# Kernel tuning notes

Hardware: AMD Instinct MI355X
Metric: run time of the kernel (lower is better)

The kernel has to match this reference:

```python
import jax, jax.numpy as jnp
import numpy as np

ND, NG, E = 25000, 20000, 1_000_000
DIN_D, DIN_G, H, OUT = 128, 128, 128, 128


def setup_inputs() -> dict:
    key = jax.random.key(0)
    ks = jax.random.split(key, 12)

    def w(k, i, o):
        return jax.random.normal(k, (i, o), jnp.float32) / np.float32(np.sqrt(i))

    return {
        "x_disease": jax.random.normal(ks[0], (ND, DIN_D), jnp.float32),
        "x_gene": jax.random.normal(ks[1], (NG, DIN_G), jnp.float32),
        "src": jax.random.randint(ks[2], (E,), 0, ND, dtype=jnp.int32),  # disease endpoint
        "dst": jax.random.randint(ks[3], (E,), 0, NG, dtype=jnp.int32),  # gene endpoint
        # layer 1, relation disease->gene: lin_l acts on aggregated disease feats, lin_r on gene feats
        "w1_dg_l": w(ks[4], DIN_D, H), "b1_dg": jnp.zeros((H,), jnp.float32), "w1_dg_r": w(ks[5], DIN_G, H),
        # layer 1, relation gene->disease (reverse edges)
        "w1_gd_l": w(ks[6], DIN_G, H), "b1_gd": jnp.zeros((H,), jnp.float32), "w1_gd_r": w(ks[7], DIN_D, H),
        # layer 2
        "w2_dg_l": w(ks[8], H, OUT), "b2_dg": jnp.zeros((OUT,), jnp.float32), "w2_dg_r": w(ks[9], H, OUT),
        "w2_gd_l": w(ks[10], H, OUT), "b2_gd": jnp.zeros((OUT,), jnp.float32), "w2_gd_r": w(ks[11], H, OUT),
    }


def _sage(x_src, x_dst, e_src, e_dst, n_dst, W_l, b_l, W_r):
    """Bipartite SAGEConv: lin_l(mean of source neighbors) + lin_r(x_dst)."""
    msg = x_src[e_src]                                         # [E, d] gather
    s = jax.ops.segment_sum(msg, e_dst, num_segments=n_dst)    # [n_dst, d]
    cnt = jax.ops.segment_sum(jnp.ones((e_dst.shape[0],), x_src.dtype),
                              e_dst, num_segments=n_dst)
    mean = s / jnp.maximum(cnt, 1.0)[:, None]                  # isolated nodes -> 0
    return mean @ W_l + b_l + x_dst @ W_r


def reference(x_disease, x_gene, src, dst,
              w1_dg_l, b1_dg, w1_dg_r, w1_gd_l, b1_gd, w1_gd_r,
              w2_dg_l, b2_dg, w2_dg_r, w2_gd_l, b2_gd, w2_gd_r):
    # HeteroConv aggr='sum': each node type receives from exactly one relation here,
    # so the cross-relation sum is the single relation output.
    g1 = _sage(x_disease, x_gene, src, dst, NG, w1_dg_l, b1_dg, w1_dg_r)   # gene <- disease
    d1 = _sage(x_gene, x_disease, dst, src, ND, w1_gd_l, b1_gd, w1_gd_r)   # disease <- gene (rev)
    g2 = _sage(d1, g1, src, dst, NG, w2_dg_l, b2_dg, w2_dg_r)
    d2 = _sage(g1, d1, dst, src, ND, w2_gd_l, b2_gd, w2_gd_r)
    return d2, g2
```

## Files before the change

kernel.cpp:

```cpp
#include <hip/hip_runtime.h>
#include <hip/hip_fp16.h>

#define ND 25000
#define NG 20000
#define NTOT (ND + NG)
#define NBLK 128
#define PREPB 1024
#define NSB 176
#define AGG_SLOTS 1563
#define AGG_GRID (8 * AGG_SLOTS)

typedef _Float16 half8 __attribute__((ext_vector_type(8)));
typedef float f32x4 __attribute__((ext_vector_type(4)));
typedef float f32x2 __attribute__((ext_vector_type(2)));

#define OFF_CNT    0ull
#define OFF_ROW    180224ull
#define OFF_PARTD  360704ull
#define OFF_PARTG  6760704ull
#define OFF_COL    11880704ull
#define OFF_WSW    15880704ull
#define OFF_XDH    16142848ull
#define OFF_XGH    22542848ull
#define OFF_X8D    27662848ull
#define OFF_X8G    30862848ull
#define OFF_MDH    33422848ull
#define OFF_MGH    39822848ull
#define OFF_D1H    44942848ull
#define OFF_G1H    51342848ull
#define OFF_D18    56462848ull
#define OFF_G18    59662848ull

struct WPtrs { const float* w[8]; };

__global__ __launch_bounds__(256) void prep_hist(const float* __restrict__ xd,
                                                 const float* __restrict__ xg,
                                                 __half* __restrict__ ydh,
                                                 __half* __restrict__ ygh,
                                                 unsigned char* __restrict__ y8d,
                                                 unsigned char* __restrict__ y8g,
                                                 WPtrs wp, _Float16* __restrict__ wsw,
                                                 const int* __restrict__ src,
                                                 const int* __restrict__ dst,
                                                 unsigned short* __restrict__ partD,
                                                 unsigned short* __restrict__ partG,
                                                 unsigned int* __restrict__ flags, int E) {
    __shared__ unsigned int h[12544];
    int bx = blockIdx.x, t = threadIdx.x;
    if (bx < 2 * NBLK) {
        bool isD = bx < NBLK;
        int bb = isD ? bx : bx - NBLK;
        const int* key = isD ? src : dst;
        int nw = isD ? (ND / 2) : (NG / 2);
        for (int i = t; i < nw; i += 256) h[i] = 0;
        __syncthreads();
        int e0 = (int)(((long long)E * bb) / NBLK);
        int e1 = (int)(((long long)E * (bb + 1)) / NBLK);
        for (int e = e0 + t; e < e1; e += 256) {
            int k = key[e];
            atomicAdd(&h[k >> 1], 1u << ((k & 1) * 16));
        }
        __syncthreads();
        unsigned int* po = (unsigned int*)((isD ? partD : partG) + (size_t)bb * (isD ? ND : NG));
        for (int i = t; i < nw; i += 256) po[i] = h[i];
        return;
    }
    int pb = bx - 2 * NBLK;
    if (pb < 8) {
        const float* W = wp.w[pb];
        _Float16* o = wsw + (size_t)pb * 16384;
        for (int rep = 0; rep < 8; ++rep) {
            int slot = rep * 256 + t;
            int lane = slot & 63, grp = slot >> 6;
            int kc = grp & 3, ntile = grp >> 2;
            int nn = ntile * 16 + (lane & 15);
            int kb = kc * 32 + (lane >> 4) * 8;
            half8 v;
#pragma unroll
            for (int j = 0; j < 8; ++j) v[j] = (_Float16)W[(size_t)(kb + j) * 128 + nn];
            *(half8*)(o + (size_t)slot * 8) = v;
        }
    } else if (pb == 8 && t < NSB) {
        flags[t] = 0u;
    }
    const int ndq = ND * 32;
    const int tot = ndq + NG * 32;
    for (int i = pb * 256 + t; i < tot; i += PREPB * 256) {
        const float* x;
        __half* y;
        unsigned char* y8;
        int idx;
        if (i < ndq) { x = xd; y = ydh; y8 = y8d; idx = i; }
        else         { x = xg; y = ygh; y8 = y8g; idx = i - ndq; }
        float4 v = ((const float4*)x)[idx];
        ((__half2*)y)[idx * 2 + 0] = __floats2half2_rn(v.x, v.y);
        ((__half2*)y)[idx * 2 + 1] = __floats2half2_rn(v.z, v.w);
        int p8 = __builtin_amdgcn_cvt_pk_fp8_f32(v.x, v.y, 0, false);
        p8 = __builtin_amdgcn_cvt_pk_fp8_f32(v.z, v.w, p8, true);
        ((int*)y8)[idx] = p8;
    }
}

__global__ __launch_bounds__(256) void scanall(unsigned short* __restrict__ partD,
                                               unsigned short* __restrict__ partG,
                                               int* __restrict__ row,
                                               unsigned int* __restrict__ flags, int E) {
    __shared__ int sd[256];
    __shared__ int sbase;
    int t = threadIdx.x, bid = blockIdx.x;
    int k = bid * 256 + t;
    int run = 0;
    if (k < NTOT) {
        unsigned short* part;
        int nb, kk;
        if (k < ND) { part = partD; nb = ND; kk = k; }
        else        { part = partG; nb = NG; kk = k - ND; }
#pragma unroll 8
        for (int b = 0; b < NBLK; ++b) {
            size_t idx = (size_t)b * nb + kk;
            int v = part[idx];
            part[idx] = (unsigned short)run;
            run += v;
        }
    }
    int tsum = run;
    sd[t] = tsum;
    __syncthreads();
    for (int off = 1; off < 256; off <<= 1) {
        int x = (t >= off) ? sd[t - off] : 0;
        __syncthreads();
        sd[t] += x;
        __syncthreads();
    }
    if (t == 0) {
        unsigned int agg = (unsigned int)sd[255] + 1u;
        __hip_atomic_store(&flags[bid], agg, __ATOMIC_RELEASE, __HIP_MEMORY_SCOPE_AGENT);
    }
    if (t < 64) {
        int s = 0;
        for (int i = t; i < bid; i += 64) {
            unsigned int v;
            do {
                v = __hip_atomic_load(&flags[i], __ATOMIC_ACQUIRE, __HIP_MEMORY_SCOPE_AGENT);
            } while (v == 0u);
            s += (int)v - 1;
        }
#pragma unroll
        for (int off = 1; off < 64; off <<= 1) s += __shfl_xor(s, off, 64);
        if (t == 0) sbase = s;
    }
    __syncthreads();
    int base = sbase;
    if (k < NTOT) row[k] = base + sd[t] - tsum;
    if (bid == 0 && t == 0) row[NTOT] = 2 * E;
}

__global__ __launch_bounds__(256) void fill2(const int* __restrict__ src,
                                             const int* __restrict__ dst,
                                             const int* __restrict__ row,
                                             const unsigned short* __restrict__ partD,
                                             const unsigned short* __restrict__ partG,
                                             unsigned short* __restrict__ col, int E) {
    __shared__ unsigned int h[12544];
    int t = threadIdx.x, b = blockIdx.x;
    bool isD = b < NBLK;
    int bb = isD ? b : b - NBLK;
    const int* key = isD ? src : dst;
    const int* val = isD ? dst : src;
    const int* rowp = isD ? row : row + ND;
    int nw = isD ? (ND / 2) : (NG / 2);
    const unsigned int* pi =
        (const unsigned int*)((isD ? partD : partG) + (size_t)bb * (isD ? ND : NG));
    for (int i = t; i < nw; i += 256) h[i] = pi[i];
    __syncthreads();
    int e0 = (int)(((long long)E * bb) / NBLK);
    int e1 = (int)(((long long)E * (bb + 1)) / NBLK);
    for (int e = e0 + t; e < e1; e += 256) {
        int k = key[e];
        int v = val[e];
        unsigned int old = atomicAdd(&h[k >> 1], 1u << ((k & 1) * 16));
        int rank = (old >> ((k & 1) * 16)) & 0xffff;
        col[rowp[k] + rank] = (unsigned short)v;
    }
}

__global__ __launch_bounds__(256, 8) void agg8m(const unsigned char* __restrict__ Xg,
                                                const unsigned char* __restrict__ Xd,
                                                const int* __restrict__ row,
                                                const unsigned short* __restrict__ col,
                                                __half* __restrict__ outd,
                                                __half* __restrict__ outg) {
    int wid = threadIdx.x >> 6, lane = threadIdx.x & 63;
    int bid = blockIdx.x;
    int xcd = bid & 7, slot = bid >> 3;
    const unsigned char* X;
    _Float16* out;
    int node, nloc;
    if (xcd < 4) {
        int db = slot * 4 + xcd;
        node = db * 4 + wid;
        if (node >= ND) return;
        X = Xg; out = (_Float16*)outd; nloc = node;
    } else {
        int gb = slot * 4 + (xcd - 4);
        int gn = gb * 4 + wid;
        if (gn >= NG) return;
        node = ND + gn;
        X = Xd; out = (_Float16*)outg; nloc = gn;
    }
    int b = row[node], e = row[node + 1];
    int g = lane >> 3, f = lane & 7;
    float acc[16];
#pragma unroll
    for (int k = 0; k < 16; ++k) acc[k] = 0.f;
    int j = b + g;
    for (; j + 8 < e; j += 16) {
        int c0 = col[j], c1 = col[j + 8];
        int4 w0 = *(const int4*)(X + (size_t)c0 * 128 + f * 16);
        int4 w1 = *(const int4*)(X + (size_t)c1 * 128 + f * 16);
        const int* wa = (const int*)&w0;
        const int* wb = (const int*)&w1;
#pragma unroll
        for (int q = 0; q < 4; ++q) {
            f32x2 l0 = __builtin_amdgcn_cvt_pk_f32_fp8(wa[q], false);
            f32x2 h0 = __builtin_amdgcn_cvt_pk_f32_fp8(wa[q], true);
            f32x2 l1 = __builtin_amdgcn_cvt_pk_f32_fp8(wb[q], false);
            f32x2 h1 = __builtin_amdgcn_cvt_pk_f32_fp8(wb[q], true);
            acc[q * 4 + 0] += l0[0] + l1[0];
            acc[q * 4 + 1] += l0[1] + l1[1];
            acc[q * 4 + 2] += h0[0] + h1[0];
            acc[q * 4 + 3] += h0[1] + h1[1];
        }
    }
    if (j < e) {
        int c = col[j];
        int4 w = *(const int4*)(X + (size_t)c * 128 + f * 16);
        const int* wa = (const int*)&w;
#pragma unroll
        for (int q = 0; q < 4; ++q) {
            f32x2 l = __builtin_amdgcn_cvt_pk_f32_fp8(wa[q], false);
            f32x2 h = __builtin_amdgcn_cvt_pk_f32_fp8(wa[q], true);
            acc[q * 4 + 0] += l[0];
            acc[q * 4 + 1] += l[1];
            acc[q * 4 + 2] += h[0];
            acc[q * 4 + 3] += h[1];
        }
    }
#pragma unroll
    for (int k = 0; k < 16; ++k) {
        acc[k] += __shfl_xor(acc[k], 8, 64);
        acc[k] += __shfl_xor(acc[k], 16, 64);
        acc[k] += __shfl_xor(acc[k], 32, 64);
    }
    if (g == 0) {
        int deg = e - b;
        float r = 1.0f / (float)(deg > 0 ? deg : 1);
        half8 o0, o1;
#pragma unroll
        for (int k = 0; k < 8; ++k) o0[k] = (_Float16)(acc[k] * r);
#pragma unroll
        for (int k = 0; k < 8; ++k) o1[k] = (_Float16)(acc[8 + k] * r);
        _Float16* op = out + (size_t)nloc * 128 + f * 16;
        *(half8*)op = o0;
        *(half8*)(op + 8) = o1;
    }
}

struct GemmDual {
    const __half *A1d, *A2d, *A1g, *A2g;
    const _Float16 *W1d, *W2d, *W1g, *W2g;
    const float *biasd, *biasg;
    float *Yfd, *Yfg;
    __half *Yhd, *Yhg;
    unsigned char *Y8d, *Y8g;
};
__global__ __launch_bounds__(256) void gemm2(GemmDual p, int nblkD, int layer) {
    int bx = blockIdx.x;
    bool isD = bx < nblkD;
    const __half* A1 = isD ? p.A1d : p.A1g;
    const __half* A2 = isD ? p.A2d : p.A2g;
    const _Float16* W1 = isD ? p.W1d : p.W1g;
    const _Float16* W2 = isD ? p.W2d : p.W2g;
    const float* bias = isD ? p.biasd : p.biasg;
    float* Yf = isD ? p.Yfd : p.Yfg;
    __half* Yh = isD ? p.Yhd : p.Yhg;
    unsigned char* Y8 = isD ? p.Y8d : p.Y8g;
    int n = isD ? ND : NG, b0 = isD ? bx : bx - nblkD;
    int t = threadIdx.x;
    int wave = t >> 6, lane = t & 63;
    int row0 = b0 * 64 + wave * 16;
    if (row0 >= n) return;
    int m = lane & 15, quad = lane >> 4;
    int arow = row0 + m;
    if (arow >= n) arow = n - 1;
    const _Float16* a1p = (const _Float16*)A1 + (size_t)arow * 128 + quad * 8;
    const _Float16* a2p = (const _Float16*)A2 + (size_t)arow * 128 + quad * 8;
    half8 a1[4], a2[4];
#pragma unroll
    for (int kc = 0; kc < 4; ++kc) {
        a1[kc] = *(const half8*)(a1p + kc * 32);
        a2[kc] = *(const half8*)(a2p + kc * 32);
    }
#pragma unroll
    for (int ntile = 0; ntile < 8; ++ntile) {
        f32x4 acc = {0.f, 0.f, 0.f, 0.f};
#pragma unroll
        for (int kc = 0; kc < 4; ++kc) {
            half8 b1 = *(const half8*)(W1 + (size_t)((ntile * 4 + kc) * 64 + lane) * 8);
            acc = __builtin_amdgcn_mfma_f32_16x16x32_f16(a1[kc], b1, acc, 0, 0, 0);
            half8 b2 = *(const half8*)(W2 + (size_t)((ntile * 4 + kc) * 64 + lane) * 8);
            acc = __builtin_amdgcn_mfma_f32_16x16x32_f16(a2[kc], b2, acc, 0, 0, 0);
        }
        int colx = ntile * 16 + m;
        float bb = bias[colx];
#pragma unroll
        for (int r = 0; r < 4; ++r) {
            int rr = row0 + quad * 4 + r;
            if (rr < n) {
                float v = acc[r] + bb;
                if (layer == 2) {
                    Yf[(size_t)rr * 128 + colx] = v;
                } else {
                    Yh[(size_t)rr * 128 + colx] = __float2half(v);
                    int p8 = __builtin_amdgcn_cvt_pk_fp8_f32(v, v, 0, false);
                    Y8[(size_t)rr * 128 + colx] = (unsigned char)(p8 & 0xff);
                }
            }
        }
    }
}

extern "C" void kernel_launch(void* const* d_in, const int* in_sizes, int n_in,
                              void* d_out, int out_size, void* d_ws, size_t ws_size,
                              hipStream_t stream) {
    const float* x_d = (const float*)d_in[0];
    const float* x_g = (const float*)d_in[1];
    const int*   src = (const int*)d_in[2];
    const int*   dst = (const int*)d_in[3];
    float* out = (float*)d_out;

    char* ws = (char*)d_ws;
    unsigned int*   flags = (unsigned int*)(ws + OFF_CNT);
    int*            row   = (int*)(ws + OFF_ROW);
    unsigned short* partD = (unsigned short*)(ws + OFF_PARTD);
    unsigned short* partG = (unsigned short*)(ws + OFF_PARTG);
    unsigned short* col   = (unsigned short*)(ws + OFF_COL);
    _Float16*       wsw   = (_Float16*)(ws + OFF_WSW);
    __half*         xd_h  = (__half*)(ws + OFF_XDH);
    __half*         xg_h  = (__half*)(ws + OFF_XGH);
    unsigned char*  x8d   = (unsigned char*)(ws + OFF_X8D);
    unsigned char*  x8g   = (unsigned char*)(ws + OFF_X8G);
    __half*         md_h  = (__half*)(ws + OFF_MDH);
    __half*         mg_h  = (__half*)(ws + OFF_MGH);
    __half*         d1_h  = (__half*)(ws + OFF_D1H);
    __half*         g1_h  = (__half*)(ws + OFF_G1H);
    unsigned char*  d1_8  = (unsigned char*)(ws + OFF_D18);
    unsigned char*  g1_8  = (unsigned char*)(ws + OFF_G18);

    const int E = in_sizes[2];
    const int nblkD = (ND + 63) / 64;
    const int nblkG = (NG + 63) / 64;

    WPtrs wp;
    wp.w[0] = (const float*)d_in[4];
    wp.w[1] = (const float*)d_in[6];
    wp.w[2] = (const float*)d_in[7];
    wp.w[3] = (const float*)d_in[9];
    wp.w[4] = (const float*)d_in[10];
    wp.w[5] = (const float*)d_in[12];
    wp.w[6] = (const float*)d_in[13];
    wp.w[7] = (const float*)d_in[15];
    const float* b1_dg = (const float*)d_in[5];
    const float* b1_gd = (const float*)d_in[8];
    const float* b2_dg = (const float*)d_in[11];
    const float* b2_gd = (const float*)d_in[14];

    prep_hist<<<2 * NBLK + PREPB, 256, 0, stream>>>(x_d, x_g, xd_h, xg_h, x8d, x8g,
                                                    wp, wsw, src, dst, partD, partG, flags, E);
    scanall<<<NSB, 256, 0, stream>>>(partD, partG, row, flags, E);
    fill2<<<2 * NBLK, 256, 0, stream>>>(src, dst, row, partD, partG, col, E);

    agg8m<<<AGG_GRID, 256, 0, stream>>>(x8g, x8d, row, col, md_h, mg_h);
    GemmDual g1p;
    g1p.A1d = md_h; g1p.A2d = xd_h; g1p.W1d = wsw + 2 * 16384; g1p.W2d = wsw + 3 * 16384;
    g1p.biasd = b1_gd; g1p.Yfd = nullptr; g1p.Yhd = d1_h; g1p.Y8d = d1_8;
    g1p.A1g = mg_h; g1p.A2g = xg_h; g1p.W1g = wsw + 0 * 16384; g1p.W2g = wsw + 1 * 16384;
    g1p.biasg = b1_dg; g1p.Yfg = nullptr; g1p.Yhg = g1_h; g1p.Y8g = g1_8;
    gemm2<<<nblkD + nblkG, 256, 0, stream>>>(g1p, nblkD, 1);

    agg8m<<<AGG_GRID, 256, 0, stream>>>(g1_8, d1_8, row, col, md_h, mg_h);
    GemmDual g2p;
    g2p.A1d = md_h; g2p.A2d = d1_h; g2p.W1d = wsw + 6 * 16384; g2p.W2d = wsw + 7 * 16384;
    g2p.biasd = b2_gd; g2p.Yfd = out; g2p.Yhd = nullptr; g2p.Y8d = nullptr;
    g2p.A1g = mg_h; g2p.A2g = g1_h; g2p.W1g = wsw + 4 * 16384; g2p.W2g = wsw + 5 * 16384;
    g2p.biasg = b2_dg; g2p.Yfg = out + (size_t)ND * 128; g2p.Yhg = nullptr; g2p.Y8g = nullptr;
    gemm2<<<nblkD + nblkG, 256, 0, stream>>>(g2p, nblkD, 2);
}
```

Measured before the change: 252.4 us.

## Fuse pipeline into two persistent cooperative kernels with grid-wide syncs

Merges the seven launches (histogram/prep, scan, fill, two aggregations, two GEMMs) into two cooperative persistent kernels separated by grid.sync barriers. Aggregation becomes a grid-stride loop over nodes instead of one block per node group. The aim is to cut kernel launch gaps and tail effects between stages. The cost is a fixed grid size bounded by occupancy, which may lower parallelism, add grid-barrier overhead, and leave some blocks idle during GEMM phases; a non-cooperative fallback path is kept.

```diff
diff --git a/kernel.cpp b/kernel.cpp
--- a/kernel.cpp
+++ b/kernel.cpp
@@ -1,14 +1,17 @@
 #include <hip/hip_runtime.h>
 #include <hip/hip_fp16.h>
+#include <hip/hip_cooperative_groups.h>
+
+namespace cg = cooperative_groups;
 
 #define ND 25000
 #define NG 20000
 #define NTOT (ND + NG)
 #define NBLK 128
-#define PREPB 1024
 #define NSB 176
-#define AGG_SLOTS 1563
-#define AGG_GRID (8 * AGG_SLOTS)
+#define NBD 391
+#define NBG 313
+#define NBT (NBD + NBG)
 
 typedef _Float16 half8 __attribute__((ext_vector_type(8)));
 typedef float f32x4 __attribute__((ext_vector_type(4)));
@@ -31,90 +34,96 @@
 #define OFF_D18    56462848ull
 #define OFF_G18    59662848ull
 
-struct WPtrs { const float* w[8]; };
-
-__global__ __launch_bounds__(256) void prep_hist(const float* __restrict__ xd,
-                                                 const float* __restrict__ xg,
-                                                 __half* __restrict__ ydh,
-                                                 __half* __restrict__ ygh,
-                                                 unsigned char* __restrict__ y8d,
-                                                 unsigned char* __restrict__ y8g,
-                                                 WPtrs wp, _Float16* __restrict__ wsw,
-                                                 const int* __restrict__ src,
-                                                 const int* __restrict__ dst,
-                                                 unsigned short* __restrict__ partD,
-                                                 unsigned short* __restrict__ partG,
-                                                 unsigned int* __restrict__ flags, int E) {
-    __shared__ unsigned int h[12544];
+struct PrepP {
+    const float *xd, *xg;
+    __half *ydh, *ygh;
+    unsigned char *y8d, *y8g;
+    const float* w[8];
+    _Float16* wsw;
+    const int *src, *dst;
+    unsigned short *partD, *partG;
+    unsigned int* flags;
+    int* row;
+    unsigned short* col;
+    int E;
+};
+
+struct MainP {
+    const unsigned char *x8d, *x8g;
+    unsigned char *d18, *g18;
+    const __half *xdh, *xgh;
+    __half *mdh, *mgh, *d1h, *g1h;
+    const _Float16* wsw;
+    const float *b1dg, *b1gd, *b2dg, *b2gd;
+    float* out;
+    const int* row;
+    const unsigned short* col;
+};
+
+
+__device__ void phase_hist_prep(const PrepP& p, unsigned int* h) {
     int bx = blockIdx.x, t = threadIdx.x;
     if (bx < 2 * NBLK) {
         bool isD = bx < NBLK;
         int bb = isD ? bx : bx - NBLK;
-        const int* key = isD ? src : dst;
+        const int* key = isD ? p.src : p.dst;
         int nw = isD ? (ND / 2) : (NG / 2);
         for (int i = t; i < nw; i += 256) h[i] = 0;
         __syncthreads();
-        int e0 = (int)(((long long)E * bb) / NBLK);
-        int e1 = (int)(((long long)E * (bb + 1)) / NBLK);
+        int e0 = (int)(((long long)p.E * bb) / NBLK);
+        int e1 = (int)(((long long)p.E * (bb + 1)) / NBLK);
         for (int e = e0 + t; e < e1; e += 256) {
             int k = key[e];
             atomicAdd(&h[k >> 1], 1u << ((k & 1) * 16));
         }
         __syncthreads();
-        unsigned int* po = (unsigned int*)((isD ? partD : partG) + (size_t)bb * (isD ? ND : NG));
+        unsigned int* po = (unsigned int*)((isD ? p.partD : p.partG) + (size_t)bb * (isD ? ND : NG));
         for (int i = t; i < nw; i += 256) po[i] = h[i];
-        return;
-    }
-    int pb = bx - 2 * NBLK;
-    if (pb < 8) {
-        const float* W = wp.w[pb];
-        _Float16* o = wsw + (size_t)pb * 16384;
-        for (int rep = 0; rep < 8; ++rep) {
-            int slot = rep * 256 + t;
-            int lane = slot & 63, grp = slot >> 6;
-            int kc = grp & 3, ntile = grp >> 2;
-            int nn = ntile * 16 + (lane & 15);
-            int kb = kc * 32 + (lane >> 4) * 8;
-            half8 v;
-#pragma unroll
-            for (int j = 0; j < 8; ++j) v[j] = (_Float16)W[(size_t)(kb + j) * 128 + nn];
-            *(half8*)(o + (size_t)slot * 8) = v;
-        }
-    } else if (pb == 8 && t < NSB) {
-        flags[t] = 0u;
-    }
-    const int ndq = ND * 32;
-    const int tot = ndq + NG * 32;
-    for (int i = pb * 256 + t; i < tot; i += PREPB * 256) {
-        const float* x;
-        __half* y;
-        unsigned char* y8;
-        int idx;
-        if (i < ndq) { x = xd; y = ydh; y8 = y8d; idx = i; }
-        else         { x = xg; y = ygh; y8 = y8g; idx = i - ndq; }
-        float4 v = ((const float4*)x)[idx];
-        ((__half2*)y)[idx * 2 + 0] = __floats2half2_rn(v.x, v.y);
-        ((__half2*)y)[idx * 2 + 1] = __floats2half2_rn(v.z, v.w);
-        int p8 = __builtin_amdgcn_cvt_pk_fp8_f32(v.x, v.y, 0, false);
-        p8 = __builtin_amdgcn_cvt_pk_fp8_f32(v.z, v.w, p8, true);
-        ((int*)y8)[idx] = p8;
-    }
-}
-
-__global__ __launch_bounds__(256) void scanall(unsigned short* __restrict__ partD,
-                                               unsigned short* __restrict__ partG,
-                                               int* __restrict__ row,
-                                               unsigned int* __restrict__ flags, int E) {
-    __shared__ int sd[256];
-    __shared__ int sbase;
+    } else {
+        int pb = bx - 2 * NBLK;
+        int ncb = gridDim.x - 2 * NBLK;
+        if (pb < 8) {
+            const float* W = p.w[pb];
+            _Float16* o = p.wsw + (size_t)pb * 16384;
+            for (int rep = 0; rep < 8; ++rep) {
+                int slot = rep * 256 + t;
+                int lane = slot & 63, grp = slot >> 6;
+                int kc = grp & 3, ntile = grp >> 2;
+                int nn = ntile * 16 + (lane & 15);
+                int kb = kc * 32 + (lane >> 4) * 8;
+                half8 v;
+#pragma unroll
+                for (int j = 0; j < 8; ++j) v[j] = (_Float16)W[(size_t)(kb + j) * 128 + nn];
+                *(half8*)(o + (size_t)slot * 8) = v;
+            }
+        } else if (pb == 8 && t < NSB) {
+            p.flags[t] = 0u;
+        }
+        const int ndq = ND * 32;
+        const int tot = ndq + NG * 32;
+        for (int i = pb * 256 + t; i < tot; i += ncb * 256) {
+            const float* x; __half* y; unsigned char* y8; int idx;
+            if (i < ndq) { x = p.xd; y = p.ydh; y8 = p.y8d; idx = i; }
+            else         { x = p.xg; y = p.ygh; y8 = p.y8g; idx = i - ndq; }
+            float4 v = ((const float4*)x)[idx];
+            ((__half2*)y)[idx * 2 + 0] = __floats2half2_rn(v.x, v.y);
+            ((__half2*)y)[idx * 2 + 1] = __floats2half2_rn(v.z, v.w);
+            int p8 = __builtin_amdgcn_cvt_pk_fp8_f32(v.x, v.y, 0, false);
+            p8 = __builtin_amdgcn_cvt_pk_fp8_f32(v.z, v.w, p8, true);
+            ((int*)y8)[idx] = p8;
+        }
+    }
+}
+
+__device__ void phase_scan(const PrepP& p, int* sd, int* sbase_p) {
     int t = threadIdx.x, bid = blockIdx.x;
     int k = bid * 256 + t;
     int run = 0;
     if (k < NTOT) {
         unsigned short* part;
         int nb, kk;
-        if (k < ND) { part = partD; nb = ND; kk = k; }
-        else        { part = partG; nb = NG; kk = k - ND; }
+        if (k < ND) { part = p.partD; nb = ND; kk = k; }
+        else        { part = p.partG; nb = NG; kk = k - ND; }
 #pragma unroll 8
         for (int b = 0; b < NBLK; ++b) {
             size_t idx = (size_t)b * nb + kk;
@@ -134,80 +143,54 @@
     }
     if (t == 0) {
         unsigned int agg = (unsigned int)sd[255] + 1u;
-        __hip_atomic_store(&flags[bid], agg, __ATOMIC_RELEASE, __HIP_MEMORY_SCOPE_AGENT);
+        __hip_atomic_store(&p.flags[bid], agg, __ATOMIC_RELEASE, __HIP_MEMORY_SCOPE_AGENT);
     }
     if (t < 64) {
         int s = 0;
         for (int i = t; i < bid; i += 64) {
             unsigned int v;
             do {
-                v = __hip_atomic_load(&flags[i], __ATOMIC_ACQUIRE, __HIP_MEMORY_SCOPE_AGENT);
+                v = __hip_atomic_load(&p.flags[i], __ATOMIC_ACQUIRE, __HIP_MEMORY_SCOPE_AGENT);
             } while (v == 0u);
             s += (int)v - 1;
         }
 #pragma unroll
         for (int off = 1; off < 64; off <<= 1) s += __shfl_xor(s, off, 64);
-        if (t == 0) sbase = s;
+        if (t == 0) *sbase_p = s;
     }
     __syncthreads();
-    int base = sbase;
-    if (k < NTOT) row[k] = base + sd[t] - tsum;
-    if (bid == 0 && t == 0) row[NTOT] = 2 * E;
-}
-
-__global__ __launch_bounds__(256) void fill2(const int* __restrict__ src,
-                                             const int* __restrict__ dst,
-                                             const int* __restrict__ row,
-                                             const unsigned short* __restrict__ partD,
-                                             const unsigned short* __restrict__ partG,
-                                             unsigned short* __restrict__ col, int E) {
-    __shared__ unsigned int h[12544];
+    int base = *sbase_p;
+    if (k < NTOT) p.row[k] = base + sd[t] - tsum;
+    if (bid == 0 && t == 0) p.row[NTOT] = 2 * p.E;
+}
+
+__device__ void phase_fill(const PrepP& p, unsigned int* h) {
     int t = threadIdx.x, b = blockIdx.x;
     bool isD = b < NBLK;
     int bb = isD ? b : b - NBLK;
-    const int* key = isD ? src : dst;
-    const int* val = isD ? dst : src;
-    const int* rowp = isD ? row : row + ND;
+    const int* key = isD ? p.src : p.dst;
+    const int* val = isD ? p.dst : p.src;
+    const int* rowp = isD ? p.row : p.row + ND;
     int nw = isD ? (ND / 2) : (NG / 2);
     const unsigned int* pi =
-        (const unsigned int*)((isD ? partD : partG) + (size_t)bb * (isD ? ND : NG));
+        (const unsigned int*)((isD ? p.partD : p.partG) + (size_t)bb * (isD ? ND : NG));
     for (int i = t; i < nw; i += 256) h[i] = pi[i];
     __syncthreads();
-    int e0 = (int)(((long long)E * bb) / NBLK);
-    int e1 = (int)(((long long)E * (bb + 1)) / NBLK);
+    int e0 = (int)(((long long)p.E * bb) / NBLK);
+    int e1 = (int)(((long long)p.E * (bb + 1)) / NBLK);
     for (int e = e0 + t; e < e1; e += 256) {
         int k = key[e];
         int v = val[e];
         unsigned int old = atomicAdd(&h[k >> 1], 1u << ((k & 1) * 16));
         int rank = (old >> ((k & 1) * 16)) & 0xffff;
-        col[rowp[k] + rank] = (unsigned short)v;
-    }
-}
-
-__global__ __launch_bounds__(256, 8) void agg8m(const unsigned char* __restrict__ Xg,
-                                                const unsigned char* __restrict__ Xd,
-                                                const int* __restrict__ row,
-                                                const unsigned short* __restrict__ col,
-                                                __half* __restrict__ outd,
-                                                __half* __restrict__ outg) {
-    int wid = threadIdx.x >> 6, lane = threadIdx.x & 63;
-    int bid = blockIdx.x;
-    int xcd = bid & 7, slot = bid >> 3;
-    const unsigned char* X;
-    _Float16* out;
-    int node, nloc;
-    if (xcd < 4) {
-        int db = slot * 4 + xcd;
-        node = db * 4 + wid;
-        if (node >= ND) return;
-        X = Xg; out = (_Float16*)outd; nloc = node;
-    } else {
-        int gb = slot * 4 + (xcd - 4);
-        int gn = gb * 4 + wid;
-        if (gn >= NG) return;
-        node = ND + gn;
-        X = Xd; out = (_Float16*)outg; nloc = gn;
-    }
+        p.col[rowp[k] + rank] = (unsigned short)v;
+    }
+}
+
+__device__ __forceinline__ void agg_one(const unsigned char* __restrict__ X,
+                                        const int* __restrict__ row,
+                                        const unsigned short* __restrict__ col,
+                                        int node, _Float16* __restrict__ op0, int lane) {
     int b = row[node], e = row[node + 1];
     int g = lane >> 3, f = lane & 7;
     float acc[16];
@@ -260,32 +243,34 @@
         for (int k = 0; k < 8; ++k) o0[k] = (_Float16)(acc[k] * r);
 #pragma unroll
         for (int k = 0; k < 8; ++k) o1[k] = (_Float16)(acc[8 + k] * r);
-        _Float16* op = out + (size_t)nloc * 128 + f * 16;
-        *(half8*)op = o0;
-        *(half8*)(op + 8) = o1;
-    }
-}
-
-struct GemmDual {
-    const __half *A1d, *A2d, *A1g, *A2g;
-    const _Float16 *W1d, *W2d, *W1g, *W2g;
-    const float *biasd, *biasg;
-    float *Yfd, *Yfg;
-    __half *Yhd, *Yhg;
-    unsigned char *Y8d, *Y8g;
-};
-__global__ __launch_bounds__(256) void gemm2(GemmDual p, int nblkD, int layer) {
-    int bx = blockIdx.x;
-    bool isD = bx < nblkD;
-    const __half* A1 = isD ? p.A1d : p.A1g;
-    const __half* A2 = isD ? p.A2d : p.A2g;
-    const _Float16* W1 = isD ? p.W1d : p.W1g;
-    const _Float16* W2 = isD ? p.W2d : p.W2g;
-    const float* bias = isD ? p.biasd : p.biasg;
-    float* Yf = isD ? p.Yfd : p.Yfg;
-    __half* Yh = isD ? p.Yhd : p.Yhg;
-    unsigned char* Y8 = isD ? p.Y8d : p.Y8g;
-    int n = isD ? ND : NG, b0 = isD ? bx : bx - nblkD;
+        *(half8*)(op0 + f * 16) = o0;
+        *(half8*)(op0 + f * 16 + 8) = o1;
+    }
+}
+
+__device__ void aggp(const unsigned char* __restrict__ Xg, const unsigned char* __restrict__ Xd,
+                     const int* __restrict__ row, const unsigned short* __restrict__ col,
+                     __half* __restrict__ outd, __half* __restrict__ outg) {
+    int wid = threadIdx.x >> 6, lane = threadIdx.x & 63;
+    int bid = blockIdx.x;
+    int xcd = bid & 7, slot = bid >> 3;
+    int stride = gridDim.x * 2;
+    if (xcd < 4) {
+        int widx = (slot * 4 + xcd) * 4 + wid;
+        for (int nd = widx; nd < ND; nd += stride)
+            agg_one(Xg, row, col, nd, (_Float16*)outd + (size_t)nd * 128, lane);
+    } else {
+        int widx = (slot * 4 + (xcd - 4)) * 4 + wid;
+        for (int gn = widx; gn < NG; gn += stride)
+            agg_one(Xd, row, col, ND + gn, (_Float16*)outg + (size_t)gn * 128, lane);
+    }
+}
+
+__device__ void gemm_tile(const __half* __restrict__ A1, const __half* __restrict__ A2,
+                          const _Float16* __restrict__ W1, const _Float16* __restrict__ W2,
+                          const float* __restrict__ bias,
+                          float* __restrict__ Yf, __half* __restrict__ Yh,
+                          unsigned char* __restrict__ Y8, int n, int b0, int layer) {
     int t = threadIdx.x;
     int wave = t >> 6, lane = t & 63;
     int row0 = b0 * 64 + wave * 16;
@@ -330,6 +315,79 @@
     }
 }
 
+__device__ void gemm_sel(const MainP& p, int layer) {
+    int bx = blockIdx.x;
+    bool isD = bx < NBD;
+    int n = isD ? ND : NG, b0 = isD ? bx : bx - NBD;
+    const __half* A1 = isD ? p.mdh : p.mgh;
+    const __half* A2;
+    const _Float16 *W1, *W2;
+    const float* bias;
+    float* Yf = nullptr;
+    __half* Yh = nullptr;
+    unsigned char* Y8 = nullptr;
+    if (layer == 1) {
+        A2 = isD ? p.xdh : p.xgh;
+        W1 = p.wsw + (size_t)(isD ? 2 : 0) * 16384;
+        W2 = p.wsw + (size_t)(isD ? 3 : 1) * 16384;
+        bias = isD ? p.b1gd : p.b1dg;
+        Yh = isD ? p.d1h : p.g1h;
+        Y8 = isD ? p.d18 : p.g18;
+    } else {
+        A2 = isD ? p.d1h : p.g1h;
+        W1 = p.wsw + (size_t)(isD ? 6 : 4) * 16384;
+        W2 = p.wsw + (size_t)(isD ? 7 : 5) * 16384;
+        bias = isD ? p.b2gd : p.b2dg;
+        Yf = isD ? p.out : p.out + (size_t)ND * 128;
+    }
+    gemm_tile(A1, A2, W1, W2, bias, Yf, Yh, Y8, n, b0, layer);
+}
+
+
+__global__ __launch_bounds__(256, 3) void csrprep(PrepP p) {
+    __shared__ unsigned int h[12544];
+    __shared__ int sbase;
+    cg::grid_group grid = cg::this_grid();
+    phase_hist_prep(p, h);
+    grid.sync();
+    if (blockIdx.x < NSB) phase_scan(p, (int*)h, &sbase);
+    grid.sync();
+    if (blockIdx.x < 2 * NBLK) phase_fill(p, h);
+}
+
+__global__ __launch_bounds__(256, 8) void mainfused(MainP p) {
+    cg::grid_group grid = cg::this_grid();
+    aggp(p.x8g, p.x8d, p.row, p.col, p.mdh, p.mgh);
+    grid.sync();
+    if (blockIdx.x < NBT) gemm_sel(p, 1);
+    grid.sync();
+    aggp(p.g18, p.d18, p.row, p.col, p.mdh, p.mgh);
+    grid.sync();
+    if (blockIdx.x < NBT) gemm_sel(p, 2);
+}
+
+
+__global__ __launch_bounds__(256) void k_prep(PrepP p) {
+    __shared__ unsigned int h[12544];
+    phase_hist_prep(p, h);
+}
+__global__ __launch_bounds__(256) void k_scan(PrepP p) {
+    __shared__ int sd[256];
+    __shared__ int sbase;
+    phase_scan(p, sd, &sbase);
+}
+__global__ __launch_bounds__(256) void k_fill(PrepP p) {
+    __shared__ unsigned int h[12544];
+    if (blockIdx.x < 2 * NBLK) phase_fill(p, h);
+}
+__global__ __launch_bounds__(256, 8) void k_agg(MainP p, int layer) {
+    if (layer == 1) aggp(p.x8g, p.x8d, p.row, p.col, p.mdh, p.mgh);
+    else            aggp(p.g18, p.d18, p.row, p.col, p.mdh, p.mgh);
+}
+__global__ __launch_bounds__(256) void k_gemm(MainP p, int layer) {
+    if (blockIdx.x < NBT) gemm_sel(p, layer);
+}
+
 extern "C" void kernel_launch(void* const* d_in, const int* in_sizes, int n_in,
                               void* d_out, int out_size, void* d_ws, size_t ws_size,
                               hipStream_t stream) {
@@ -340,59 +398,85 @@
     float* out = (float*)d_out;
 
     char* ws = (char*)d_ws;
-    unsigned int*   flags = (unsigned int*)(ws + OFF_CNT);
-    int*            row   = (int*)(ws + OFF_ROW);
-    unsigned short* partD = (unsigned short*)(ws + OFF_PARTD);
-    unsigned short* partG = (unsigned short*)(ws + OFF_PARTG);
-    unsigned short* col   = (unsigned short*)(ws + OFF_COL);
-    _Float16*       wsw   = (_Float16*)(ws + OFF_WSW);
-    __half*         xd_h  = (__half*)(ws + OFF_XDH);
-    __half*         xg_h  = (__half*)(ws + OFF_XGH);
-    unsigned char*  x8d   = (unsigned char*)(ws + OFF_X8D);
-    unsigned char*  x8g   = (unsigned char*)(ws + OFF_X8G);
-    __half*         md_h  = (__half*)(ws + OFF_MDH);
-    __half*         mg_h  = (__half*)(ws + OFF_MGH);
-    __half*         d1_h  = (__half*)(ws + OFF_D1H);
-    __half*         g1_h  = (__half*)(ws + OFF_G1H);
-    unsigned char*  d1_8  = (unsigned char*)(ws + OFF_D18);
-    unsigned char*  g1_8  = (unsigned char*)(ws + OFF_G18);
-
-    const int E = in_sizes[2];
-    const int nblkD = (ND + 63) / 64;
-    const int nblkG = (NG + 63) / 64;
-
-    WPtrs wp;
-    wp.w[0] = (const float*)d_in[4];
-    wp.w[1] = (const float*)d_in[6];
-    wp.w[2] = (const float*)d_in[7];
-    wp.w[3] = (const float*)d_in[9];
-    wp.w[4] = (const float*)d_in[10];
-    wp.w[5] = (const float*)d_in[12];
-    wp.w[6] = (const float*)d_in[13];
-    wp.w[7] = (const float*)d_in[15];
-    const float* b1_dg = (const float*)d_in[5];
-    const float* b1_gd = (const float*)d_in[8];
-    const float* b2_dg = (const float*)d_in[11];
-    const float* b2_gd = (const float*)d_in[14];
-
-    prep_hist<<<2 * NBLK + PREPB, 256, 0, stream>>>(x_d, x_g, xd_h, xg_h, x8d, x8g,
-                                                    wp, wsw, src, dst, partD, partG, flags, E);
-    scanall<<<NSB, 256, 0, stream>>>(partD, partG, row, flags, E);
-    fill2<<<2 * NBLK, 256, 0, stream>>>(src, dst, row, partD, partG, col, E);
-
-    agg8m<<<AGG_GRID, 256, 0, stream>>>(x8g, x8d, row, col, md_h, mg_h);
-    GemmDual g1p;
-    g1p.A1d = md_h; g1p.A2d = xd_h; g1p.W1d = wsw + 2 * 16384; g1p.W2d = wsw + 3 * 16384;
-    g1p.biasd = b1_gd; g1p.Yfd = nullptr; g1p.Yhd = d1_h; g1p.Y8d = d1_8;
-    g1p.A1g = mg_h; g1p.A2g = xg_h; g1p.W1g = wsw + 0 * 16384; g1p.W2g = wsw + 1 * 16384;
-    g1p.biasg = b1_dg; g1p.Yfg = nullptr; g1p.Yhg = g1_h; g1p.Y8g = g1_8;
-    gemm2<<<nblkD + nblkG, 256, 0, stream>>>(g1p, nblkD, 1);
-
-    agg8m<<<AGG_GRID, 256, 0, stream>>>(g1_8, d1_8, row, col, md_h, mg_h);
-    GemmDual g2p;
-    g2p.A1d = md_h; g2p.A2d = d1_h; g2p.W1d = wsw + 6 * 16384; g2p.W2d = wsw + 7 * 16384;
-    g2p.biasd = b2_gd; g2p.Yfd = out; g2p.Yhd = nullptr; g2p.Y8d = nullptr;
-    g2p.A1g = mg_h; g2p.A2g = g1_h; g2p.W1g = wsw + 4 * 16384; g2p.W2g = wsw + 5 * 16384;
-    g2p.biasg = b2_dg; g2p.Yfg = out + (size_t)ND * 128; g2p.Yhg = nullptr; g2p.Y8g = nullptr;
-    gemm2<<<nblkD + nblkG, 256, 0, stream>>>(g2p, nblkD, 2);
-}
+    PrepP pp;
+    pp.xd = x_d; pp.xg = x_g;
+    pp.ydh = (__half*)(ws + OFF_XDH); pp.ygh = (__half*)(ws + OFF_XGH);
+    pp.y8d = (unsigned char*)(ws + OFF_X8D); pp.y8g = (unsigned char*)(ws + OFF_X8G);
+    pp.w[0] = (const float*)d_in[4];
+    pp.w[1] = (const float*)d_in[6];
+    pp.w[2] = (const float*)d_in[7];
+    pp.w[3] = (const float*)d_in[9];
+    pp.w[4] = (const float*)d_in[10];
+    pp.w[5] = (const float*)d_in[12];
+    pp.w[6] = (const float*)d_in[13];
+    pp.w[7] = (const float*)d_in[15];
+    pp.wsw = (_Float16*)(ws + OFF_WSW);
+    pp.src = src; pp.dst = dst;
+    pp.partD = (unsigned short*)(ws + OFF_PARTD);
+    pp.partG = (unsigned short*)(ws + OFF_PARTG);
+    pp.flags = (unsigned int*)(ws + OFF_CNT);
+    pp.row = (int*)(ws + OFF_ROW);
+    pp.col = (unsigned short*)(ws + OFF_COL);
+    pp.E = in_sizes[2];
+
+    MainP mp;
+    mp.x8d = (const unsigned char*)(ws + OFF_X8D);
+    mp.x8g = (const unsigned char*)(ws + OFF_X8G);
+    mp.d18 = (unsigned char*)(ws + OFF_D18);
+    mp.g18 = (unsigned char*)(ws + OFF_G18);
+    mp.xdh = (const __half*)(ws + OFF_XDH);
+    mp.xgh = (const __half*)(ws + OFF_XGH);
+    mp.mdh = (__half*)(ws + OFF_MDH);
+    mp.mgh = (__half*)(ws + OFF_MGH);
+    mp.d1h = (__half*)(ws + OFF_D1H);
+    mp.g1h = (__half*)(ws + OFF_G1H);
+    mp.wsw = (const _Float16*)(ws + OFF_WSW);
+    mp.b1dg = (const float*)d_in[5];
+    mp.b1gd = (const float*)d_in[8];
+    mp.b2dg = (const float*)d_in[11];
+    mp.b2gd = (const float*)d_in[14];
+    mp.out = out;
+    mp.row = (const int*)(ws + OFF_ROW);
+    mp.col = (const unsigned short*)(ws + OFF_COL);
+
+    static int coop = -1, gA = 0, gB = 0;
+    if (coop < 0) {
+        int ca = 0, dev = 0;
+        hipGetDevice(&dev);
+        hipDeviceGetAttribute(&ca, hipDeviceAttributeCooperativeLaunch, dev);
+        if (ca) {
+            int mA = 0, mB = 0;
+            hipOccupancyMaxActiveBlocksPerMultiprocessor(&mA, csrprep, 256, 0);
+            hipOccupancyMaxActiveBlocksPerMultiprocessor(&mB, mainfused, 256, 0);
+            hipDeviceProp_t prop;
+            hipGetDeviceProperties(&prop, dev);
+            int ncu = prop.multiProcessorCount;
+            gA = mA * ncu; if (gA > 768) gA = 768;
+            gB = (mB * ncu) & ~7; if (gB > 2048) gB = 2048;
+            coop = (gA >= 2 * NBLK + 9 && gB >= NBT) ? 1 : 0;
+        } else {
+            coop = 0;
+        }
+    }
+
+    if (coop) {
+        void* aA[] = { (void*)&pp };
+        void* aB[] = { (void*)&mp };
+        hipError_t e1 = hipLaunchCooperativeKernel((const void*)csrprep, dim3(gA), dim3(256),
+                                                   aA, 0, stream);
+        hipError_t e2 = (e1 == hipSuccess)
+            ? hipLaunchCooperativeKernel((const void*)mainfused, dim3(gB), dim3(256),
+                                         aB, 0, stream)
+            : e1;
+        if (e1 == hipSuccess && e2 == hipSuccess) return;
+        coop = 0;
+    }
+
+    k_prep<<<2 * NBLK + 1024, 256, 0, stream>>>(pp);
+    k_scan<<<NSB, 256, 0, stream>>>(pp);
+    k_fill<<<2 * NBLK, 256, 0, stream>>>(pp);
+    k_agg<<<2048, 256, 0, stream>>>(mp, 1);
+    k_gemm<<<NBT, 256, 0, stream>>>(mp, 1);
+    k_agg<<<2048, 256, 0, stream>>>(mp, 2);
+    k_gemm<<<NBT, 256, 0, stream>>>(mp, 2);
+}
```

Result: slower. 912.8 us (+261.6%).

## Replace per-block histogram CSR build with global atomic counts and fused scan-fill

Applied to the files above, without the earlier changes.

Removes the per-block partial histograms (128 blocks × nodes of ushort partials) and their serial scan. Degrees are now counted with global atomics, and a single kernel scans them and then fills col through global atomic cursors after a grid-wide barrier. This cuts large partial-buffer traffic and one launch, but adds global atomic contention. It also makes the within-row neighbor order nondeterministic. The grid barrier relies on all 1024 blocks being co-resident.

```diff
diff --git a/kernel.cpp b/kernel.cpp
--- a/kernel.cpp
+++ b/kernel.cpp
@@ -4,9 +4,10 @@
 #define ND 25000
 #define NG 20000
 #define NTOT (ND + NG)
-#define NBLK 128
+#define HB 128
 #define PREPB 1024
 #define NSB 176
+#define CFB 1024
 #define AGG_SLOTS 1563
 #define AGG_GRID (8 * AGG_SLOTS)
 
@@ -16,8 +17,8 @@
 
 #define OFF_CNT    0ull
 #define OFF_ROW    180224ull
-#define OFF_PARTD  360704ull
-#define OFF_PARTG  6760704ull
+#define OFF_FLG    360704ull
+#define OFF_POS    361728ull
 #define OFF_COL    11880704ull
 #define OFF_WSW    15880704ull
 #define OFF_XDH    16142848ull
@@ -33,6 +34,13 @@
 
 struct WPtrs { const float* w[8]; };
 
+__global__ __launch_bounds__(256) void zerok(int* __restrict__ cnt,
+                                             unsigned int* __restrict__ flags) {
+    int i = blockIdx.x * 256 + threadIdx.x;
+    for (int k = i; k < NTOT; k += gridDim.x * 256) cnt[k] = 0;
+    if (i <= NSB) flags[i] = 0u;
+}
+
 __global__ __launch_bounds__(256) void prep_hist(const float* __restrict__ xd,
                                                  const float* __restrict__ xg,
                                                  __half* __restrict__ ydh,
@@ -42,30 +50,18 @@
                                                  WPtrs wp, _Float16* __restrict__ wsw,
                                                  const int* __restrict__ src,
                                                  const int* __restrict__ dst,
-                                                 unsigned short* __restrict__ partD,
-                                                 unsigned short* __restrict__ partG,
-                                                 unsigned int* __restrict__ flags, int E) {
-    __shared__ unsigned int h[12544];
+                                                 int* __restrict__ cnt, int E) {
     int bx = blockIdx.x, t = threadIdx.x;
-    if (bx < 2 * NBLK) {
-        bool isD = bx < NBLK;
-        int bb = isD ? bx : bx - NBLK;
-        const int* key = isD ? src : dst;
-        int nw = isD ? (ND / 2) : (NG / 2);
-        for (int i = t; i < nw; i += 256) h[i] = 0;
-        __syncthreads();
-        int e0 = (int)(((long long)E * bb) / NBLK);
-        int e1 = (int)(((long long)E * (bb + 1)) / NBLK);
+    if (bx < HB) {
+        int e0 = (int)(((long long)E * bx) / HB);
+        int e1 = (int)(((long long)E * (bx + 1)) / HB);
         for (int e = e0 + t; e < e1; e += 256) {
-            int k = key[e];
-            atomicAdd(&h[k >> 1], 1u << ((k & 1) * 16));
-        }
-        __syncthreads();
-        unsigned int* po = (unsigned int*)((isD ? partD : partG) + (size_t)bb * (isD ? ND : NG));
-        for (int i = t; i < nw; i += 256) po[i] = h[i];
+            atomicAdd(&cnt[src[e]], 1);
+            atomicAdd(&cnt[ND + dst[e]], 1);
+        }
         return;
     }
-    int pb = bx - 2 * NBLK;
+    int pb = bx - HB;
     if (pb < 8) {
         const float* W = wp.w[pb];
         _Float16* o = wsw + (size_t)pb * 16384;
@@ -80,8 +76,6 @@
             for (int j = 0; j < 8; ++j) v[j] = (_Float16)W[(size_t)(kb + j) * 128 + nn];
             *(half8*)(o + (size_t)slot * 8) = v;
         }
-    } else if (pb == 8 && t < NSB) {
-        flags[t] = 0u;
     }
     const int ndq = ND * 32;
     const int tot = ndq + NG * 32;
@@ -101,86 +95,68 @@
     }
 }
 
-__global__ __launch_bounds__(256) void scanall(unsigned short* __restrict__ partD,
-                                               unsigned short* __restrict__ partG,
-                                               int* __restrict__ row,
-                                               unsigned int* __restrict__ flags, int E) {
+__global__ __launch_bounds__(256) void csrfin(const int* __restrict__ cnt,
+                                              int* __restrict__ row,
+                                              int* __restrict__ pos,
+                                              unsigned int* __restrict__ flags,
+                                              const int* __restrict__ src,
+                                              const int* __restrict__ dst,
+                                              unsigned short* __restrict__ col, int E) {
     __shared__ int sd[256];
     __shared__ int sbase;
     int t = threadIdx.x, bid = blockIdx.x;
-    int k = bid * 256 + t;
-    int run = 0;
-    if (k < NTOT) {
-        unsigned short* part;
-        int nb, kk;
-        if (k < ND) { part = partD; nb = ND; kk = k; }
-        else        { part = partG; nb = NG; kk = k - ND; }
-#pragma unroll 8
-        for (int b = 0; b < NBLK; ++b) {
-            size_t idx = (size_t)b * nb + kk;
-            int v = part[idx];
-            part[idx] = (unsigned short)run;
-            run += v;
-        }
-    }
-    int tsum = run;
-    sd[t] = tsum;
+    if (bid < NSB) {
+        int k = bid * 256 + t;
+        int tsum = (k < NTOT) ? cnt[k] : 0;
+        sd[t] = tsum;
+        __syncthreads();
+        for (int off = 1; off < 256; off <<= 1) {
+            int x = (t >= off) ? sd[t - off] : 0;
+            __syncthreads();
+            sd[t] += x;
+            __syncthreads();
+        }
+        if (t == 0) {
+            __hip_atomic_store(&flags[bid], (unsigned int)sd[255] + 1u,
+                               __ATOMIC_RELEASE, __HIP_MEMORY_SCOPE_AGENT);
+        }
+        if (t < 64) {
+            int s = 0;
+            for (int i = t; i < bid; i += 64) {
+                unsigned int v;
+                do {
+                    v = __hip_atomic_load(&flags[i], __ATOMIC_ACQUIRE, __HIP_MEMORY_SCOPE_AGENT);
+                } while (v == 0u);
+                s += (int)v - 1;
+            }
+#pragma unroll
+            for (int off = 1; off < 64; off <<= 1) s += __shfl_xor(s, off, 64);
+            if (t == 0) sbase = s;
+        }
+        __syncthreads();
+        if (k < NTOT) {
+            int r = sbase + sd[t] - tsum;
+            row[k] = r;
+            pos[k] = r;
+        }
+        if (bid == 0 && t == 0) row[NTOT] = 2 * E;
+        __syncthreads();
+        if (t == 0)
+            __hip_atomic_fetch_add((int*)&flags[NSB], 1,
+                                   __ATOMIC_RELEASE, __HIP_MEMORY_SCOPE_AGENT);
+    }
+    if (t == 0) {
+        while (__hip_atomic_load((int*)&flags[NSB], __ATOMIC_ACQUIRE,
+                                 __HIP_MEMORY_SCOPE_AGENT) < NSB)
+            __builtin_amdgcn_s_sleep(2);
+    }
     __syncthreads();
-    for (int off = 1; off < 256; off <<= 1) {
-        int x = (t >= off) ? sd[t - off] : 0;
-        __syncthreads();
-        sd[t] += x;
-        __syncthreads();
-    }
-    if (t == 0) {
-        unsigned int agg = (unsigned int)sd[255] + 1u;
-        __hip_atomic_store(&flags[bid], agg, __ATOMIC_RELEASE, __HIP_MEMORY_SCOPE_AGENT);
-    }
-    if (t < 64) {
-        int s = 0;
-        for (int i = t; i < bid; i += 64) {
-            unsigned int v;
-            do {
-                v = __hip_atomic_load(&flags[i], __ATOMIC_ACQUIRE, __HIP_MEMORY_SCOPE_AGENT);
-            } while (v == 0u);
-            s += (int)v - 1;
-        }
-#pragma unroll
-        for (int off = 1; off < 64; off <<= 1) s += __shfl_xor(s, off, 64);
-        if (t == 0) sbase = s;
-    }
-    __syncthreads();
-    int base = sbase;
-    if (k < NTOT) row[k] = base + sd[t] - tsum;
-    if (bid == 0 && t == 0) row[NTOT] = 2 * E;
-}
-
-__global__ __launch_bounds__(256) void fill2(const int* __restrict__ src,
-                                             const int* __restrict__ dst,
-                                             const int* __restrict__ row,
-                                             const unsigned short* __restrict__ partD,
-                                             const unsigned short* __restrict__ partG,
-                                             unsigned short* __restrict__ col, int E) {
-    __shared__ unsigned int h[12544];
-    int t = threadIdx.x, b = blockIdx.x;
-    bool isD = b < NBLK;
-    int bb = isD ? b : b - NBLK;
-    const int* key = isD ? src : dst;
-    const int* val = isD ? dst : src;
-    const int* rowp = isD ? row : row + ND;
-    int nw = isD ? (ND / 2) : (NG / 2);
-    const unsigned int* pi =
-        (const unsigned int*)((isD ? partD : partG) + (size_t)bb * (isD ? ND : NG));
-    for (int i = t; i < nw; i += 256) h[i] = pi[i];
-    __syncthreads();
-    int e0 = (int)(((long long)E * bb) / NBLK);
-    int e1 = (int)(((long long)E * (bb + 1)) / NBLK);
-    for (int e = e0 + t; e < e1; e += 256) {
-        int k = key[e];
-        int v = val[e];
-        unsigned int old = atomicAdd(&h[k >> 1], 1u << ((k & 1) * 16));
-        int rank = (old >> ((k & 1) * 16)) & 0xffff;
-        col[rowp[k] + rank] = (unsigned short)v;
+    for (int i = bid * 256 + t; i < 2 * E; i += CFB * 256) {
+        int k, v;
+        if (i < E) { k = src[i];            v = dst[i]; }
+        else       { int j = i - E; k = ND + dst[j]; v = src[j]; }
+        int p = atomicAdd(&pos[k], 1);
+        col[p] = (unsigned short)v;
     }
 }
 
@@ -340,10 +316,10 @@
     float* out = (float*)d_out;
 
     char* ws = (char*)d_ws;
-    unsigned int*   flags = (unsigned int*)(ws + OFF_CNT);
+    int*            cnt   = (int*)(ws + OFF_CNT);
     int*            row   = (int*)(ws + OFF_ROW);
-    unsigned short* partD = (unsigned short*)(ws + OFF_PARTD);
-    unsigned short* partG = (unsigned short*)(ws + OFF_PARTG);
+    unsigned int*   flags = (unsigned int*)(ws + OFF_FLG);
+    int*            pos   = (int*)(ws + OFF_POS);
     unsigned short* col   = (unsigned short*)(ws + OFF_COL);
     _Float16*       wsw   = (_Float16*)(ws + OFF_WSW);
     __half*         xd_h  = (__half*)(ws + OFF_XDH);
@@ -375,10 +351,10 @@
     const float* b2_dg = (const float*)d_in[11];
     const float* b2_gd = (const float*)d_in[14];
 
-    prep_hist<<<2 * NBLK + PREPB, 256, 0, stream>>>(x_d, x_g, xd_h, xg_h, x8d, x8g,
-                                                    wp, wsw, src, dst, partD, partG, flags, E);
-    scanall<<<NSB, 256, 0, stream>>>(partD, partG, row, flags, E);
-    fill2<<<2 * NBLK, 256, 0, stream>>>(src, dst, row, partD, partG, col, E);
+    zerok<<<64, 256, 0, stream>>>(cnt, flags);
+    prep_hist<<<HB + PREPB, 256, 0, stream>>>(x_d, x_g, xd_h, xg_h, x8d, x8g,
+                                              wp, wsw, src, dst, cnt, E);
+    csrfin<<<CFB, 256, 0, stream>>>(cnt, row, pos, flags, src, dst, col, E);
 
     agg8m<<<AGG_GRID, 256, 0, stream>>>(x8g, x8d, row, col, md_h, mg_h);
     GemmDual g1p;
```

New measurement: 482.2 us. 1.91x slower.

## Partition CSR fill and aggregation by node range per XCD

Applied to the files above, without the earlier changes.

The CSR fill kernel is split into 8 node-range partitions, each mapped to one XCD (bid&7), so each block keeps only its range's write cursors in shared memory and scatters col entries for keys in that range. The aggregation kernel maps nodes to XCDs by contiguous ranges instead of interleaving, so col/row data written by a given XCD is reused from its L2. The intent is better L2 locality across fill and aggregation and smaller LDS use per block. In exchange every fill block scans its whole edge slice, which reads the edge list four times over and skips most edges.

```diff
diff --git a/kernel.cpp b/kernel.cpp
--- a/kernel.cpp
+++ b/kernel.cpp
@@ -7,6 +7,8 @@
 #define NBLK 128
 #define PREPB 1024
 #define NSB 176
+#define DRNG 6250
+#define GRNG 5000
 #define AGG_SLOTS 1563
 #define AGG_GRID (8 * AGG_SLOTS)
 
@@ -155,32 +157,33 @@
     if (bid == 0 && t == 0) row[NTOT] = 2 * E;
 }
 
-__global__ __launch_bounds__(256) void fill2(const int* __restrict__ src,
-                                             const int* __restrict__ dst,
-                                             const int* __restrict__ row,
-                                             const unsigned short* __restrict__ partD,
-                                             const unsigned short* __restrict__ partG,
-                                             unsigned short* __restrict__ col, int E) {
-    __shared__ unsigned int h[12544];
-    int t = threadIdx.x, b = blockIdx.x;
-    bool isD = b < NBLK;
-    int bb = isD ? b : b - NBLK;
-    const int* key = isD ? src : dst;
-    const int* val = isD ? dst : src;
-    const int* rowp = isD ? row : row + ND;
-    int nw = isD ? (ND / 2) : (NG / 2);
-    const unsigned int* pi =
-        (const unsigned int*)((isD ? partD : partG) + (size_t)bb * (isD ? ND : NG));
-    for (int i = t; i < nw; i += 256) h[i] = pi[i];
+__global__ __launch_bounds__(256) void fill2x(const int* __restrict__ src,
+                                              const int* __restrict__ dst,
+                                              const int* __restrict__ row,
+                                              const unsigned short* __restrict__ partD,
+                                              const unsigned short* __restrict__ partG,
+                                              unsigned short* __restrict__ col, int E) {
+    __shared__ unsigned int cur[DRNG];
+    int t = threadIdx.x, bid = blockIdx.x;
+    int x = bid & 7;
+    int s = bid >> 3;
+    bool isD = x < 4;
+    int r0, rng, nbase, nb;
+    const int *key, *val;
+    const unsigned short* part;
+    if (isD) { r0 = x * DRNG;       rng = DRNG; key = src; val = dst; part = partD; nb = ND; nbase = 0;  }
+    else     { r0 = (x - 4) * GRNG; rng = GRNG; key = dst; val = src; part = partG; nb = NG; nbase = ND; }
+    for (int i = t; i < rng; i += 256)
+        cur[i] = (unsigned int)row[nbase + r0 + i] + part[(size_t)s * nb + r0 + i];
     __syncthreads();
-    int e0 = (int)(((long long)E * bb) / NBLK);
-    int e1 = (int)(((long long)E * (bb + 1)) / NBLK);
+    int e0 = (int)(((long long)E * s) / NBLK);
+    int e1 = (int)(((long long)E * (s + 1)) / NBLK);
     for (int e = e0 + t; e < e1; e += 256) {
         int k = key[e];
-        int v = val[e];
-        unsigned int old = atomicAdd(&h[k >> 1], 1u << ((k & 1) * 16));
-        int rank = (old >> ((k & 1) * 16)) & 0xffff;
-        col[rowp[k] + rank] = (unsigned short)v;
+        if (k >= r0 && k < r0 + rng) {
+            unsigned int p = atomicAdd(&cur[k - r0], 1u);
+            col[p] = (unsigned short)val[e];
+        }
     }
 }
 
@@ -197,16 +200,19 @@
     _Float16* out;
     int node, nloc;
     if (xcd < 4) {
-        int db = slot * 4 + xcd;
-        node = db * 4 + wid;
-        if (node >= ND) return;
-        X = Xg; out = (_Float16*)outd; nloc = node;
+        int loc = slot * 4 + wid;
+        if (loc >= DRNG) return;
+        nloc = xcd * DRNG + loc;
+        if (nloc >= ND) return;
+        node = nloc;
+        X = Xg; out = (_Float16*)outd;
     } else {
-        int gb = slot * 4 + (xcd - 4);
-        int gn = gb * 4 + wid;
-        if (gn >= NG) return;
-        node = ND + gn;
-        X = Xd; out = (_Float16*)outg; nloc = gn;
+        int loc = slot * 4 + wid;
+        if (loc >= GRNG) return;
+        nloc = (xcd - 4) * GRNG + loc;
+        if (nloc >= NG) return;
+        node = ND + nloc;
+        X = Xd; out = (_Float16*)outg;
     }
     int b = row[node], e = row[node + 1];
     int g = lane >> 3, f = lane & 7;
@@ -378,7 +384,7 @@
     prep_hist<<<2 * NBLK + PREPB, 256, 0, stream>>>(x_d, x_g, xd_h, xg_h, x8d, x8g,
                                                     wp, wsw, src, dst, partD, partG, flags, E);
     scanall<<<NSB, 256, 0, stream>>>(partD, partG, row, flags, E);
-    fill2<<<2 * NBLK, 256, 0, stream>>>(src, dst, row, partD, partG, col, E);
+    fill2x<<<NBLK * 8, 256, 0, stream>>>(src, dst, row, partD, partG, col, E);
 
     agg8m<<<AGG_GRID, 256, 0, stream>>>(x8g, x8d, row, col, md_h, mg_h);
     GemmDual g1p;
```

After: 253.4 us. No clear change (+0.4%).
